# Kernel optimization log

Measured on AMD Instinct MI355X. Metric: run time of the kernel, lower is better.

## Reference

```python
import jax, jax.numpy as jnp
import numpy as np

E_DIM = 64
N_EMBED = 1024
N_TOKENS = 262144


def setup_inputs() -> dict:
    key = jax.random.key(0)
    k1, k2 = jax.random.split(key)
    inp = jax.random.normal(k1, (N_TOKENS, E_DIM), dtype=jnp.float32)
    # codebook init mirrors torch uniform_(-1/n_embed, 1/n_embed)
    embed = jax.random.uniform(k2, (E_DIM, N_EMBED), dtype=jnp.float32,
                               minval=-1.0 / N_EMBED, maxval=1.0 / N_EMBED)
    return {"input": inp, "embed": embed}


def reference(input, embed):
    e_dim, n_embed = embed.shape
    flatten = input.reshape(-1, e_dim)  # [N, e_dim]
    dist = (jnp.sum(flatten * flatten, axis=1, keepdims=True)
            - 2.0 * flatten @ embed
            + jnp.sum(embed * embed, axis=0, keepdims=True))
    embed_idxs = jnp.argmin(dist, axis=1)  # matches (-dist).max(1) indices
    embed_idxs = embed_idxs.reshape(input.shape[:-1])
    quantize = jnp.take(embed.T, embed_idxs, axis=0)  # gather codes -> [..., e_dim]
    # straight-through estimator
    quantize_input_grad = input + jax.lax.stop_gradient(quantize - input)
    return (quantize, input, quantize_input_grad, embed_idxs, embed)
```

## Files before the change

### kernel.cpp

```cpp
#include <hip/hip_runtime.h>
#include <hip/hip_bf16.h>
#include <math.h>

#define E_DIM    64
#define N_EMBED  1024
#define N_TOKENS 262144
#define FQCAP    32768

typedef __attribute__((ext_vector_type(8)))  short bf16x8;
typedef __attribute__((ext_vector_type(16))) float f32x16;


__device__ __forceinline__ short f2bf_bits(float f) {
    __hip_bfloat16 h = __float2bfloat16(f);
    return *reinterpret_cast<short*>(&h);
}
__device__ __forceinline__ float bfbits2f(short s) {
    unsigned int u = ((unsigned int)(unsigned short)s) << 16;
    return __uint_as_float(u);
}

__device__ __forceinline__ float exact_d(const float* __restrict__ xrow,
                                         const float* __restrict__ emb,
                                         const float* __restrict__ csum,
                                         float a, int j) {
#pragma clang fp contract(off)
    float b = 0.f;
#pragma unroll
    for (int k = 0; k < E_DIM; ++k) b = fmaf(xrow[k], emb[k * N_EMBED + j], b);
    return (a - 2.0f * b) + csum[j];
}

__device__ __forceinline__ float a_np_of(const float* x) {
#pragma clang fp contract(off)
    float s[16];
#pragma unroll
    for (int i = 0; i < 16; ++i)
        s[i] = (x[i] * x[i] + x[i + 16] * x[i + 16]) +
               (x[i + 32] * x[i + 32] + x[i + 48] * x[i + 48]);
    float hh[8];
#pragma unroll
    for (int i = 0; i < 8; ++i) hh[i] = s[i] + s[i + 8];
    float uu[4];
#pragma unroll
    for (int i = 0; i < 4; ++i) uu[i] = hh[i] + hh[i + 4];
    return (uu[0] + uu[2]) + (uu[1] + uu[3]);
}

__device__ __forceinline__ bool lexless(float av, int ai, float bv, int bi) {
    return (av < bv) || (av == bv && ai < bi);
}

__global__ __launch_bounds__(256) void vq_prep(const float* __restrict__ emb,
                                               short* __restrict__ eTc,
                                               float* __restrict__ out_e,
                                               float* __restrict__ embT,
                                               float* __restrict__ c_out) {
    const int b = blockIdx.x;
    if (b < 256) {
        const int t = b * 256 + threadIdx.x;
        const int k = t >> 10, n = t & 1023;
        float e = emb[t];
        float m2 = -2.0f * e;
        short hb = f2bf_bits(m2);
        short lb = f2bf_bits(m2 - bfbits2f(hb));
        const int chunk = n >> 7, code = n & 127, slot = k >> 3, jj = k & 7;
        const int base = chunk * 16384 + (slot * 128 + code) * 8 + jj;
        eTc[base]        = hb;
        eTc[base + 8192] = lb;
        out_e[t] = e;
        embT[n * E_DIM + k] = e;
    } else {
#pragma clang fp contract(off)
        const int j = (b - 256) * 256 + threadIdx.x;
        float e = emb[j];
        float s = e * e;
        for (int k = 1; k < E_DIM; ++k) {
            float ek = emb[k * N_EMBED + j];
            float pk = ek * ek;
            s = s + pk;
        }
        c_out[j] = s;
    }
}

__device__ __forceinline__ void tile_epilogue(
    const f32x16& acc, int codebase_global, int h,
    float& v1, float& v2, float& v3, int& i1, int& i2) {
#pragma unroll
    for (int r = 0; r < 16; ++r) {
        const int row = (r & 3) + 8 * (r >> 2) + 4 * h;
        const float d = acc[r];
        const int idx = codebase_global + row;
        if (d < v3) {
            if (d < v1)      { v3 = v2; v2 = v1; i2 = i1; v1 = d; i1 = idx; }
            else if (d < v2) { v3 = v2; v2 = d;  i2 = idx; }
            else             { v3 = d; }
        }
    }
}

__global__ __launch_bounds__(256, 4) void vq_screen_kernel(
    const float* __restrict__ in, const float* __restrict__ emb,
    const float* __restrict__ csum, const short* __restrict__ eTc,
    float* __restrict__ out_idx,
    unsigned int* __restrict__ qcnt, unsigned int* __restrict__ fullQ)
{
    __shared__ uint4 lds_e[2048];

    const int t = threadIdx.x;
    const int wave = t >> 6, l = t & 63, col = l & 31, h = l >> 5;
    const int tok = blockIdx.x * 128 + wave * 32 + col;
    const float* xrow = in + (size_t)tok * E_DIM;

    float xv[4][8];
#pragma unroll
    for (int s = 0; s < 4; ++s) {
        float4 u0 = *reinterpret_cast<const float4*>(xrow + s * 16 + h * 8);
        float4 u1 = *reinterpret_cast<const float4*>(xrow + s * 16 + h * 8 + 4);
        xv[s][0] = u0.x; xv[s][1] = u0.y; xv[s][2] = u0.z; xv[s][3] = u0.w;
        xv[s][4] = u1.x; xv[s][5] = u1.y; xv[s][6] = u1.z; xv[s][7] = u1.w;
    }
    bf16x8 bhi[4], blo[4];
    float sax_h = 0.f;
#pragma unroll
    for (int s = 0; s < 4; ++s) {
#pragma unroll
        for (int j = 0; j < 8; ++j) {
            float x = xv[s][j];
            sax_h += fabsf(x);
            short hb = f2bf_bits(x);
            bhi[s][j] = hb;
            blo[s][j] = f2bf_bits(x - bfbits2f(hb));
        }
    }
    const float sax = sax_h + __shfl_xor(sax_h, 32, 64);

    float a_np;
    {
#pragma clang fp contract(off)
        float sv[8];
#pragma unroll
        for (int j = 0; j < 8; ++j) {
            float p0 = xv[0][j] * xv[0][j];
            float p1 = xv[1][j] * xv[1][j];
            float p2 = xv[2][j] * xv[2][j];
            float p3 = xv[3][j] * xv[3][j];
            sv[j] = (p0 + p1) + (p2 + p3);
        }
        float hh[8];
#pragma unroll
        for (int j = 0; j < 8; ++j) hh[j] = sv[j] + __shfl_xor(sv[j], 32, 64);
        float u0 = hh[0] + hh[4], u1 = hh[1] + hh[5];
        float u2 = hh[2] + hh[6], u3 = hh[3] + hh[7];
        a_np = (u0 + u2) + (u1 + u3);
    }

    float v1 = 3.4e38f, v2 = 3.4e38f, v3 = 3.4e38f;
    int i1 = 0, i2 = 0;

    for (int cc = 0; cc < 8; ++cc) {
        __syncthreads();
        {
            const uint4* gsrc = reinterpret_cast<const uint4*>(eTc) + cc * 2048;
#pragma unroll
            for (int j = 0; j < 8; ++j) lds_e[j * 256 + t] = gsrc[j * 256 + t];
        }
        __syncthreads();

        const int cb = cc << 7;
#pragma unroll
        for (int tp = 0; tp < 2; ++tp) {
            const int c0 = tp * 64 + col;
            const int cbase = cb + tp * 64 + 4 * h;
            const float4 cA0 = *reinterpret_cast<const float4*>(&csum[cbase + 0]);
            const float4 cA1 = *reinterpret_cast<const float4*>(&csum[cbase + 8]);
            const float4 cA2 = *reinterpret_cast<const float4*>(&csum[cbase + 16]);
            const float4 cA3 = *reinterpret_cast<const float4*>(&csum[cbase + 24]);
            const float4 cB0 = *reinterpret_cast<const float4*>(&csum[cbase + 32]);
            const float4 cB1 = *reinterpret_cast<const float4*>(&csum[cbase + 40]);
            const float4 cB2 = *reinterpret_cast<const float4*>(&csum[cbase + 48]);
            const float4 cB3 = *reinterpret_cast<const float4*>(&csum[cbase + 56]);
            f32x16 accA, accB;
            accA[0]=cA0.x;  accA[1]=cA0.y;  accA[2]=cA0.z;  accA[3]=cA0.w;
            accA[4]=cA1.x;  accA[5]=cA1.y;  accA[6]=cA1.z;  accA[7]=cA1.w;
            accA[8]=cA2.x;  accA[9]=cA2.y;  accA[10]=cA2.z; accA[11]=cA2.w;
            accA[12]=cA3.x; accA[13]=cA3.y; accA[14]=cA3.z; accA[15]=cA3.w;
            accB[0]=cB0.x;  accB[1]=cB0.y;  accB[2]=cB0.z;  accB[3]=cB0.w;
            accB[4]=cB1.x;  accB[5]=cB1.y;  accB[6]=cB1.z;  accB[7]=cB1.w;
            accB[8]=cB2.x;  accB[9]=cB2.y;  accB[10]=cB2.z; accB[11]=cB2.w;
            accB[12]=cB3.x; accB[13]=cB3.y; accB[14]=cB3.z; accB[15]=cB3.w;
#pragma unroll
            for (int s = 0; s < 4; ++s) {
                const int slot = 2 * s + h;
                bf16x8 ahA = *reinterpret_cast<const bf16x8*>(&lds_e[slot * 128 + c0]);
                bf16x8 alA = *reinterpret_cast<const bf16x8*>(&lds_e[1024 + slot * 128 + c0]);
                bf16x8 ahB = *reinterpret_cast<const bf16x8*>(&lds_e[slot * 128 + c0 + 32]);
                bf16x8 alB = *reinterpret_cast<const bf16x8*>(&lds_e[1024 + slot * 128 + c0 + 32]);
                accA = __builtin_amdgcn_mfma_f32_32x32x16_bf16(ahA, bhi[s], accA, 0, 0, 0);
                accB = __builtin_amdgcn_mfma_f32_32x32x16_bf16(ahB, bhi[s], accB, 0, 0, 0);
                accA = __builtin_amdgcn_mfma_f32_32x32x16_bf16(ahA, blo[s], accA, 0, 0, 0);
                accB = __builtin_amdgcn_mfma_f32_32x32x16_bf16(ahB, blo[s], accB, 0, 0, 0);
                accA = __builtin_amdgcn_mfma_f32_32x32x16_bf16(alA, bhi[s], accA, 0, 0, 0);
                accB = __builtin_amdgcn_mfma_f32_32x32x16_bf16(alB, bhi[s], accB, 0, 0, 0);
            }
            tile_epilogue(accA, cb + tp * 64,      h, v1, v2, v3, i1, i2);
            tile_epilogue(accB, cb + tp * 64 + 32, h, v1, v2, v3, i1, i2);
        }
    }

    const float w1 = __shfl_xor(v1, 32, 64), w2 = __shfl_xor(v2, 32, 64), w3 = __shfl_xor(v3, 32, 64);
    const int   j1 = __shfl_xor(i1, 32, 64), j2 = __shfl_xor(i2, 32, 64);
    const bool bfirst = lexless(w1, j1, v1, i1);
    const float r1v = bfirst ? w1 : v1;  const int r1i = bfirst ? j1 : i1;
    const float cav = bfirst ? v1 : v2;  const int cai = bfirst ? i1 : i2;
    const float cbv = bfirst ? w2 : w1;  const int cbi = bfirst ? j2 : j1;
    const bool bsec = lexless(cbv, cbi, cav, cai);
    const float r2v = bsec ? cbv : cav;  const int r2i = bsec ? cbi : cai;
    const float r3v = bsec ? fminf(cav, bfirst ? w3 : w2)
                           : fminf(cbv, bfirst ? v2 : v3);

    if (l < 32) {
        const float thr = 8e-5f + 4e-7f * sax;
        const bool sane = (a_np < 150.f) && (sax < 128.f) && (fabsf(r1v) < 0.5f);
        int fin = r1i;
        if (sane && (r2v - r1v > thr)) {
        } else if (sane && (r3v - r1v > thr)) {
            const float d1 = exact_d(xrow, emb, csum, a_np, r1i);
            const float d2 = exact_d(xrow, emb, csum, a_np, r2i);
            if (d2 < d1 || (d2 == d1 && r2i < r1i)) fin = r2i;
        } else {
            const unsigned int qi = atomicAdd(qcnt, 1u);
            if (qi < FQCAP) fullQ[qi] = (unsigned int)tok;
        }
        out_idx[tok] = (float)fin;
    }
}

__global__ __launch_bounds__(256) void vq_full_kernel(
    const float* __restrict__ in, const float* __restrict__ emb,
    const float* __restrict__ csum, const unsigned int* __restrict__ qcnt,
    const unsigned int* __restrict__ fullQ, float* __restrict__ out_idx) {
#pragma clang fp contract(off)
    unsigned int nq = *qcnt;
    if (nq > FQCAP) nq = FQCAP;
    const int l = threadIdx.x & 63;
    for (unsigned int w = blockIdx.x * 4 + (threadIdx.x >> 6); w < nq; w += 1024) {
        const int tok = (int)fullQ[w];
        const float* xrow = in + (size_t)tok * E_DIM;
        float x[E_DIM];
#pragma unroll
        for (int j4 = 0; j4 < 16; ++j4) {
            const float4 u = *reinterpret_cast<const float4*>(xrow + j4 * 4);
            x[j4 * 4 + 0] = u.x; x[j4 * 4 + 1] = u.y;
            x[j4 * 4 + 2] = u.z; x[j4 * 4 + 3] = u.w;
        }
        const float a = a_np_of(x);
        const int c0 = l * 16;
        float b[16];
#pragma unroll
        for (int q = 0; q < 16; ++q) b[q] = 0.f;
        for (int k = 0; k < E_DIM; ++k) {
            const float xk = x[k];
            const float* er = emb + k * N_EMBED + c0;
#pragma unroll
            for (int q = 0; q < 16; ++q) b[q] = fmaf(xk, er[q], b[q]);
        }
        float bd = 3.4e38f; int bi = 1 << 30;
#pragma unroll
        for (int q = 0; q < 16; ++q) {
            const float d = (a - 2.0f * b[q]) + csum[c0 + q];
            if (d < bd) { bd = d; bi = c0 + q; }
        }
        for (int m = 1; m < 64; m <<= 1) {
            const float od = __shfl_xor(bd, m, 64);
            const int oi = __shfl_xor(bi, m, 64);
            if (od < bd || (od == bd && oi < bi)) { bd = od; bi = oi; }
        }
        if (l == 0) out_idx[tok] = (float)bi;
    }
}

__global__ __launch_bounds__(256) void vq_gather_kernel(
    const float* __restrict__ in, const float* __restrict__ embT,
    const float* __restrict__ idxf,
    float* __restrict__ out_q, float* __restrict__ out_in, float* __restrict__ out_g) {
#pragma clang fp contract(off)
    const size_t j = (size_t)blockIdx.x * 256 + threadIdx.x;
    const int m  = (int)(j >> 4);
    const int k0 = ((int)j & 15) * 4;
    const int idx = (int)idxf[m];

    const float4 x = reinterpret_cast<const float4*>(in)[j];
    const float4 q = *reinterpret_cast<const float4*>(&embT[(size_t)idx * E_DIM + k0]);

    float4 g;
    g.x = x.x + (q.x - x.x);
    g.y = x.y + (q.y - x.y);
    g.z = x.z + (q.z - x.z);
    g.w = x.w + (q.w - x.w);

    reinterpret_cast<float4*>(out_q)[j]  = q;
    reinterpret_cast<float4*>(out_in)[j] = x;
    reinterpret_cast<float4*>(out_g)[j]  = g;
}

extern "C" void kernel_launch(void* const* d_in, const int* in_sizes, int n_in,
                              void* d_out, int out_size, void* d_ws, size_t ws_size,
                              hipStream_t stream) {
    const float* in  = (const float*)d_in[0];
    const float* emb = (const float*)d_in[1];

    float* out     = (float*)d_out;
    float* out_q   = out;
    float* out_in  = out + (size_t)N_TOKENS * E_DIM;
    float* out_g   = out + 2ull * N_TOKENS * E_DIM;
    float* out_idx = out + 3ull * N_TOKENS * E_DIM;
    float* out_e   = out_idx + N_TOKENS;

    unsigned char* ws = (unsigned char*)d_ws;
    float*          c_ws  = (float*)(ws);
    short*          eTc   = (short*)(ws + 4096);
    float*          embT  = (float*)(ws + 4096 + 262144);
    unsigned int*   qcnt  = (unsigned int*)(ws + 4096 + 262144 + 262144);
    unsigned int*   fullQ = (unsigned int*)(ws + 4096 + 262144 + 262144 + 256);

    hipMemsetAsync(qcnt, 0, sizeof(unsigned int), stream);

    vq_prep<<<260, 256, 0, stream>>>(emb, eTc, out_e, embT, c_ws);

    vq_screen_kernel<<<N_TOKENS / 128, 256, 0, stream>>>(
        in, emb, c_ws, eTc, out_idx, qcnt, fullQ);

    vq_full_kernel<<<256, 256, 0, stream>>>(in, emb, c_ws, qcnt, fullQ, out_idx);

    const int gather_blocks = (N_TOKENS * E_DIM / 4) / 256;
    vq_gather_kernel<<<gather_blocks, 256, 0, stream>>>(in, embT, out_idx,
                                                        out_q, out_in, out_g);
}
```

Before: 273.7 us.

## Fuse gather/STE output writes into screen kernel and defer pair checks

Removes the separate gather kernel by having the screen kernel write quantize, input copy and straight-through outputs directly from registers using the screened index. Ambiguous two-candidate tokens are now queued to a new pair kernel instead of doing scalar exact checks inline, and the pair and full-rescan kernels overwrite the outputs for tokens they correct. This saves re-reading the input and the index array, at the cost of redundant writes for corrected tokens, an extra launch, and lower occupancy (launch bound 4 to 3).

```diff
diff --git a/kernel.cpp b/kernel.cpp
--- a/kernel.cpp
+++ b/kernel.cpp
@@ -5,6 +5,7 @@
 #define E_DIM    64
 #define N_EMBED  1024
 #define N_TOKENS 262144
+#define PQCAP    32768
 #define FQCAP    32768
 
 typedef __attribute__((ext_vector_type(8)))  short bf16x8;
@@ -18,17 +19,6 @@
 __device__ __forceinline__ float bfbits2f(short s) {
     unsigned int u = ((unsigned int)(unsigned short)s) << 16;
     return __uint_as_float(u);
-}
-
-__device__ __forceinline__ float exact_d(const float* __restrict__ xrow,
-                                         const float* __restrict__ emb,
-                                         const float* __restrict__ csum,
-                                         float a, int j) {
-#pragma clang fp contract(off)
-    float b = 0.f;
-#pragma unroll
-    for (int k = 0; k < E_DIM; ++k) b = fmaf(xrow[k], emb[k * N_EMBED + j], b);
-    return (a - 2.0f * b) + csum[j];
 }
 
 __device__ __forceinline__ float a_np_of(const float* x) {
@@ -100,11 +90,13 @@
     }
 }
 
-__global__ __launch_bounds__(256, 4) void vq_screen_kernel(
-    const float* __restrict__ in, const float* __restrict__ emb,
-    const float* __restrict__ csum, const short* __restrict__ eTc,
-    float* __restrict__ out_idx,
-    unsigned int* __restrict__ qcnt, unsigned int* __restrict__ fullQ)
+__global__ __launch_bounds__(256, 3) void vq_screen_kernel(
+    const float* __restrict__ in, const float* __restrict__ csum,
+    const short* __restrict__ eTc, const float* __restrict__ embT,
+    float* __restrict__ out_idx, float* __restrict__ out_q,
+    float* __restrict__ out_in, float* __restrict__ out_g,
+    unsigned int* __restrict__ qcnt,
+    uint2* __restrict__ pairQ, unsigned int* __restrict__ fullQ)
 {
     __shared__ uint4 lds_e[2048];
 
@@ -220,29 +212,105 @@
     const float r3v = bsec ? fminf(cav, bfirst ? w3 : w2)
                            : fminf(cbv, bfirst ? v2 : v3);
 
+    const float thr = 8e-5f + 4e-7f * sax;
+    const bool sane = (a_np < 150.f) && (sax < 128.f) && (fabsf(r1v) < 0.5f);
+    const int fin = r1i;
+
     if (l < 32) {
-        const float thr = 8e-5f + 4e-7f * sax;
-        const bool sane = (a_np < 150.f) && (sax < 128.f) && (fabsf(r1v) < 0.5f);
-        int fin = r1i;
         if (sane && (r2v - r1v > thr)) {
         } else if (sane && (r3v - r1v > thr)) {
-            const float d1 = exact_d(xrow, emb, csum, a_np, r1i);
-            const float d2 = exact_d(xrow, emb, csum, a_np, r2i);
-            if (d2 < d1 || (d2 == d1 && r2i < r1i)) fin = r2i;
+            const unsigned int qi = atomicAdd(&qcnt[0], 1u);
+            if (qi < PQCAP)
+                pairQ[qi] = make_uint2((unsigned int)tok,
+                                       (unsigned int)r1i | ((unsigned int)r2i << 16));
         } else {
-            const unsigned int qi = atomicAdd(qcnt, 1u);
+            const unsigned int qi = atomicAdd(&qcnt[1], 1u);
             if (qi < FQCAP) fullQ[qi] = (unsigned int)tok;
         }
         out_idx[tok] = (float)fin;
+    }
+
+    {
+        const float* qrow = embT + (size_t)fin * E_DIM;
+        const size_t obase = (size_t)tok * E_DIM;
+#pragma unroll
+        for (int s = 0; s < 4; ++s) {
+            const int k0 = s * 16 + h * 8;
+            const float4 q0 = *reinterpret_cast<const float4*>(qrow + k0);
+            const float4 q1 = *reinterpret_cast<const float4*>(qrow + k0 + 4);
+            const float4 x0 = make_float4(xv[s][0], xv[s][1], xv[s][2], xv[s][3]);
+            const float4 x1 = make_float4(xv[s][4], xv[s][5], xv[s][6], xv[s][7]);
+            float4 g0, g1;
+            g0.x = x0.x + (q0.x - x0.x); g0.y = x0.y + (q0.y - x0.y);
+            g0.z = x0.z + (q0.z - x0.z); g0.w = x0.w + (q0.w - x0.w);
+            g1.x = x1.x + (q1.x - x1.x); g1.y = x1.y + (q1.y - x1.y);
+            g1.z = x1.z + (q1.z - x1.z); g1.w = x1.w + (q1.w - x1.w);
+            *reinterpret_cast<float4*>(out_q  + obase + k0)     = q0;
+            *reinterpret_cast<float4*>(out_q  + obase + k0 + 4) = q1;
+            *reinterpret_cast<float4*>(out_in + obase + k0)     = x0;
+            *reinterpret_cast<float4*>(out_in + obase + k0 + 4) = x1;
+            *reinterpret_cast<float4*>(out_g  + obase + k0)     = g0;
+            *reinterpret_cast<float4*>(out_g  + obase + k0 + 4) = g1;
+        }
+    }
+}
+
+__global__ __launch_bounds__(256) void vq_pair_kernel(
+    const float* __restrict__ in, const float* __restrict__ emb,
+    const float* __restrict__ embT, const float* __restrict__ csum,
+    const unsigned int* __restrict__ qcnt, const uint2* __restrict__ pairQ,
+    float* __restrict__ out_idx, float* __restrict__ out_q,
+    float* __restrict__ out_g) {
+#pragma clang fp contract(off)
+    unsigned int nq = qcnt[0];
+    if (nq > PQCAP) nq = PQCAP;
+    const unsigned int i = blockIdx.x * 256 + threadIdx.x;
+    if (i >= nq) return;
+    const uint2 e = pairQ[i];
+    const int tok = (int)e.x;
+    const int c1 = (int)(e.y & 0xFFFFu), c2 = (int)(e.y >> 16);
+    const float* xrow = in + (size_t)tok * E_DIM;
+    float x[E_DIM];
+#pragma unroll
+    for (int j4 = 0; j4 < 16; ++j4) {
+        const float4 u = *reinterpret_cast<const float4*>(xrow + j4 * 4);
+        x[j4 * 4 + 0] = u.x; x[j4 * 4 + 1] = u.y;
+        x[j4 * 4 + 2] = u.z; x[j4 * 4 + 3] = u.w;
+    }
+    const float a = a_np_of(x);
+    float b1 = 0.f, b2 = 0.f;
+#pragma unroll
+    for (int k = 0; k < E_DIM; ++k) {
+        b1 = fmaf(x[k], emb[k * N_EMBED + c1], b1);
+        b2 = fmaf(x[k], emb[k * N_EMBED + c2], b2);
+    }
+    const float d1 = (a - 2.0f * b1) + csum[c1];
+    const float d2 = (a - 2.0f * b2) + csum[c2];
+    const int fin = (d2 < d1 || (d2 == d1 && c2 < c1)) ? c2 : c1;
+    out_idx[tok] = (float)fin;
+    const float* qrow = embT + (size_t)fin * E_DIM;
+    const size_t obase = (size_t)tok * E_DIM;
+#pragma unroll
+    for (int j4 = 0; j4 < 16; ++j4) {
+        const float4 q = *reinterpret_cast<const float4*>(qrow + j4 * 4);
+        float4 g;
+        g.x = x[j4 * 4 + 0] + (q.x - x[j4 * 4 + 0]);
+        g.y = x[j4 * 4 + 1] + (q.y - x[j4 * 4 + 1]);
+        g.z = x[j4 * 4 + 2] + (q.z - x[j4 * 4 + 2]);
+        g.w = x[j4 * 4 + 3] + (q.w - x[j4 * 4 + 3]);
+        *reinterpret_cast<float4*>(out_q + obase + j4 * 4) = q;
+        *reinterpret_cast<float4*>(out_g + obase + j4 * 4) = g;
     }
 }
 
 __global__ __launch_bounds__(256) void vq_full_kernel(
     const float* __restrict__ in, const float* __restrict__ emb,
-    const float* __restrict__ csum, const unsigned int* __restrict__ qcnt,
-    const unsigned int* __restrict__ fullQ, float* __restrict__ out_idx) {
-#pragma clang fp contract(off)
-    unsigned int nq = *qcnt;
+    const float* __restrict__ embT, const float* __restrict__ csum,
+    const unsigned int* __restrict__ qcnt, const unsigned int* __restrict__ fullQ,
+    float* __restrict__ out_idx, float* __restrict__ out_q,
+    float* __restrict__ out_g) {
+#pragma clang fp contract(off)
+    unsigned int nq = qcnt[1];
     if (nq > FQCAP) nq = FQCAP;
     const int l = threadIdx.x & 63;
     for (unsigned int w = blockIdx.x * 4 + (threadIdx.x >> 6); w < nq; w += 1024) {
@@ -278,31 +346,18 @@
             if (od < bd || (od == bd && oi < bi)) { bd = od; bi = oi; }
         }
         if (l == 0) out_idx[tok] = (float)bi;
-    }
-}
-
-__global__ __launch_bounds__(256) void vq_gather_kernel(
-    const float* __restrict__ in, const float* __restrict__ embT,
-    const float* __restrict__ idxf,
-    float* __restrict__ out_q, float* __restrict__ out_in, float* __restrict__ out_g) {
-#pragma clang fp contract(off)
-    const size_t j = (size_t)blockIdx.x * 256 + threadIdx.x;
-    const int m  = (int)(j >> 4);
-    const int k0 = ((int)j & 15) * 4;
-    const int idx = (int)idxf[m];
-
-    const float4 x = reinterpret_cast<const float4*>(in)[j];
-    const float4 q = *reinterpret_cast<const float4*>(&embT[(size_t)idx * E_DIM + k0]);
-
-    float4 g;
-    g.x = x.x + (q.x - x.x);
-    g.y = x.y + (q.y - x.y);
-    g.z = x.z + (q.z - x.z);
-    g.w = x.w + (q.w - x.w);
-
-    reinterpret_cast<float4*>(out_q)[j]  = q;
-    reinterpret_cast<float4*>(out_in)[j] = x;
-    reinterpret_cast<float4*>(out_g)[j]  = g;
+        if (l < 16) {
+            const float4 qv = *reinterpret_cast<const float4*>(embT + (size_t)bi * E_DIM + l * 4);
+            const float4 xq = *reinterpret_cast<const float4*>(xrow + l * 4);
+            float4 g;
+            g.x = xq.x + (qv.x - xq.x);
+            g.y = xq.y + (qv.y - xq.y);
+            g.z = xq.z + (qv.z - xq.z);
+            g.w = xq.w + (qv.w - xq.w);
+            *reinterpret_cast<float4*>(out_q + (size_t)tok * E_DIM + l * 4) = qv;
+            *reinterpret_cast<float4*>(out_g + (size_t)tok * E_DIM + l * 4) = g;
+        }
+    }
 }
 
 extern "C" void kernel_launch(void* const* d_in, const int* in_sizes, int n_in,
@@ -323,18 +378,20 @@
     short*          eTc   = (short*)(ws + 4096);
     float*          embT  = (float*)(ws + 4096 + 262144);
     unsigned int*   qcnt  = (unsigned int*)(ws + 4096 + 262144 + 262144);
-    unsigned int*   fullQ = (unsigned int*)(ws + 4096 + 262144 + 262144 + 256);
-
-    hipMemsetAsync(qcnt, 0, sizeof(unsigned int), stream);
+    uint2*          pairQ = (uint2*)(ws + 4096 + 262144 + 262144 + 256);
+    unsigned int*   fullQ = (unsigned int*)(ws + 4096 + 262144 + 262144 + 256
+                                            + (size_t)PQCAP * 8);
+
+    hipMemsetAsync(qcnt, 0, 2 * sizeof(unsigned int), stream);
 
     vq_prep<<<260, 256, 0, stream>>>(emb, eTc, out_e, embT, c_ws);
 
     vq_screen_kernel<<<N_TOKENS / 128, 256, 0, stream>>>(
-        in, emb, c_ws, eTc, out_idx, qcnt, fullQ);
-
-    vq_full_kernel<<<256, 256, 0, stream>>>(in, emb, c_ws, qcnt, fullQ, out_idx);
-
-    const int gather_blocks = (N_TOKENS * E_DIM / 4) / 256;
-    vq_gather_kernel<<<gather_blocks, 256, 0, stream>>>(in, embT, out_idx,
-                                                        out_q, out_in, out_g);
-}
+        in, c_ws, eTc, embT, out_idx, out_q, out_in, out_g, qcnt, pairQ, fullQ);
+
+    vq_pair_kernel<<<PQCAP / 256, 256, 0, stream>>>(
+        in, emb, embT, c_ws, qcnt, pairQ, out_idx, out_q, out_g);
+
+    vq_full_kernel<<<256, 256, 0, stream>>>(
+        in, emb, embT, c_ws, qcnt, fullQ, out_idx, out_q, out_g);
+}
```

Result: slower. 306.6 us (+12.0%).

## Fuse gather and straight-through outputs into screen and fallback kernels

Applied to the files above, without the earlier changes.

Removes the separate gather kernel and writes the input copy, quantized codes and straight-through gradient directly from the screening kernel using the x values already held in registers. The fallback full-search kernel then overwrites the quantized and gradient rows for the tokens it re-resolves. This avoids re-reading the input and the index array and saves a kernel launch. In exchange the screen kernel gains register pressure and stores, and queued tokens are written twice, with ordering between the two kernels relied on for correctness.

```diff
diff --git a/kernel.cpp b/kernel.cpp
--- a/kernel.cpp
+++ b/kernel.cpp
@@ -103,7 +103,9 @@
 __global__ __launch_bounds__(256, 4) void vq_screen_kernel(
     const float* __restrict__ in, const float* __restrict__ emb,
     const float* __restrict__ csum, const short* __restrict__ eTc,
-    float* __restrict__ out_idx,
+    const float* __restrict__ embT,
+    float* __restrict__ out_idx, float* __restrict__ out_q,
+    float* __restrict__ out_in, float* __restrict__ out_g,
     unsigned int* __restrict__ qcnt, unsigned int* __restrict__ fullQ)
 {
     __shared__ uint4 lds_e[2048];
@@ -112,6 +114,7 @@
     const int wave = t >> 6, l = t & 63, col = l & 31, h = l >> 5;
     const int tok = blockIdx.x * 128 + wave * 32 + col;
     const float* xrow = in + (size_t)tok * E_DIM;
+    const size_t obase = (size_t)tok * E_DIM;
 
     float xv[4][8];
 #pragma unroll
@@ -121,6 +124,16 @@
         xv[s][0] = u0.x; xv[s][1] = u0.y; xv[s][2] = u0.z; xv[s][3] = u0.w;
         xv[s][4] = u1.x; xv[s][5] = u1.y; xv[s][6] = u1.z; xv[s][7] = u1.w;
     }
+
+#pragma unroll
+    for (int s = 0; s < 4; ++s) {
+        const int k0 = s * 16 + h * 8;
+        *reinterpret_cast<float4*>(out_in + obase + k0) =
+            make_float4(xv[s][0], xv[s][1], xv[s][2], xv[s][3]);
+        *reinterpret_cast<float4*>(out_in + obase + k0 + 4) =
+            make_float4(xv[s][4], xv[s][5], xv[s][6], xv[s][7]);
+    }
+
     bf16x8 bhi[4], blo[4];
     float sax_h = 0.f;
 #pragma unroll
@@ -220,27 +233,48 @@
     const float r3v = bsec ? fminf(cav, bfirst ? w3 : w2)
                            : fminf(cbv, bfirst ? v2 : v3);
 
-    if (l < 32) {
-        const float thr = 8e-5f + 4e-7f * sax;
-        const bool sane = (a_np < 150.f) && (sax < 128.f) && (fabsf(r1v) < 0.5f);
-        int fin = r1i;
-        if (sane && (r2v - r1v > thr)) {
-        } else if (sane && (r3v - r1v > thr)) {
-            const float d1 = exact_d(xrow, emb, csum, a_np, r1i);
-            const float d2 = exact_d(xrow, emb, csum, a_np, r2i);
-            if (d2 < d1 || (d2 == d1 && r2i < r1i)) fin = r2i;
-        } else {
+    const float thr = 8e-5f + 4e-7f * sax;
+    const bool sane = (a_np < 150.f) && (sax < 128.f) && (fabsf(r1v) < 0.5f);
+    int fin = r1i;
+    if (sane && (r2v - r1v > thr)) {
+    } else if (sane && (r3v - r1v > thr)) {
+        const float d1 = exact_d(xrow, emb, csum, a_np, r1i);
+        const float d2 = exact_d(xrow, emb, csum, a_np, r2i);
+        if (d2 < d1 || (d2 == d1 && r2i < r1i)) fin = r2i;
+    } else {
+        if (l < 32) {
             const unsigned int qi = atomicAdd(qcnt, 1u);
             if (qi < FQCAP) fullQ[qi] = (unsigned int)tok;
         }
-        out_idx[tok] = (float)fin;
+    }
+    if (l < 32) out_idx[tok] = (float)fin;
+
+    {
+        const float* qrow = embT + (size_t)fin * E_DIM;
+#pragma unroll
+        for (int s = 0; s < 4; ++s) {
+            const int k0 = s * 16 + h * 8;
+            const float4 q0 = *reinterpret_cast<const float4*>(qrow + k0);
+            const float4 q1 = *reinterpret_cast<const float4*>(qrow + k0 + 4);
+            float4 g0, g1;
+            g0.x = xv[s][0] + (q0.x - xv[s][0]); g0.y = xv[s][1] + (q0.y - xv[s][1]);
+            g0.z = xv[s][2] + (q0.z - xv[s][2]); g0.w = xv[s][3] + (q0.w - xv[s][3]);
+            g1.x = xv[s][4] + (q1.x - xv[s][4]); g1.y = xv[s][5] + (q1.y - xv[s][5]);
+            g1.z = xv[s][6] + (q1.z - xv[s][6]); g1.w = xv[s][7] + (q1.w - xv[s][7]);
+            *reinterpret_cast<float4*>(out_q + obase + k0)     = q0;
+            *reinterpret_cast<float4*>(out_q + obase + k0 + 4) = q1;
+            *reinterpret_cast<float4*>(out_g + obase + k0)     = g0;
+            *reinterpret_cast<float4*>(out_g + obase + k0 + 4) = g1;
+        }
     }
 }
 
 __global__ __launch_bounds__(256) void vq_full_kernel(
     const float* __restrict__ in, const float* __restrict__ emb,
-    const float* __restrict__ csum, const unsigned int* __restrict__ qcnt,
-    const unsigned int* __restrict__ fullQ, float* __restrict__ out_idx) {
+    const float* __restrict__ embT, const float* __restrict__ csum,
+    const unsigned int* __restrict__ qcnt, const unsigned int* __restrict__ fullQ,
+    float* __restrict__ out_idx, float* __restrict__ out_q,
+    float* __restrict__ out_g) {
 #pragma clang fp contract(off)
     unsigned int nq = *qcnt;
     if (nq > FQCAP) nq = FQCAP;
@@ -278,31 +312,18 @@
             if (od < bd || (od == bd && oi < bi)) { bd = od; bi = oi; }
         }
         if (l == 0) out_idx[tok] = (float)bi;
-    }
-}
-
-__global__ __launch_bounds__(256) void vq_gather_kernel(
-    const float* __restrict__ in, const float* __restrict__ embT,
-    const float* __restrict__ idxf,
-    float* __restrict__ out_q, float* __restrict__ out_in, float* __restrict__ out_g) {
-#pragma clang fp contract(off)
-    const size_t j = (size_t)blockIdx.x * 256 + threadIdx.x;
-    const int m  = (int)(j >> 4);
-    const int k0 = ((int)j & 15) * 4;
-    const int idx = (int)idxf[m];
-
-    const float4 x = reinterpret_cast<const float4*>(in)[j];
-    const float4 q = *reinterpret_cast<const float4*>(&embT[(size_t)idx * E_DIM + k0]);
-
-    float4 g;
-    g.x = x.x + (q.x - x.x);
-    g.y = x.y + (q.y - x.y);
-    g.z = x.z + (q.z - x.z);
-    g.w = x.w + (q.w - x.w);
-
-    reinterpret_cast<float4*>(out_q)[j]  = q;
-    reinterpret_cast<float4*>(out_in)[j] = x;
-    reinterpret_cast<float4*>(out_g)[j]  = g;
+        if (l < 16) {
+            const float4 qv = *reinterpret_cast<const float4*>(embT + (size_t)bi * E_DIM + l * 4);
+            const float4 xq = *reinterpret_cast<const float4*>(xrow + l * 4);
+            float4 g;
+            g.x = xq.x + (qv.x - xq.x);
+            g.y = xq.y + (qv.y - xq.y);
+            g.z = xq.z + (qv.z - xq.z);
+            g.w = xq.w + (qv.w - xq.w);
+            *reinterpret_cast<float4*>(out_q + (size_t)tok * E_DIM + l * 4) = qv;
+            *reinterpret_cast<float4*>(out_g + (size_t)tok * E_DIM + l * 4) = g;
+        }
+    }
 }
 
 extern "C" void kernel_launch(void* const* d_in, const int* in_sizes, int n_in,
@@ -330,11 +351,8 @@
     vq_prep<<<260, 256, 0, stream>>>(emb, eTc, out_e, embT, c_ws);
 
     vq_screen_kernel<<<N_TOKENS / 128, 256, 0, stream>>>(
-        in, emb, c_ws, eTc, out_idx, qcnt, fullQ);
-
-    vq_full_kernel<<<256, 256, 0, stream>>>(in, emb, c_ws, qcnt, fullQ, out_idx);
-
-    const int gather_blocks = (N_TOKENS * E_DIM / 4) / 256;
-    vq_gather_kernel<<<gather_blocks, 256, 0, stream>>>(in, embT, out_idx,
-                                                        out_q, out_in, out_g);
-}
+        in, emb, c_ws, eTc, embT, out_idx, out_q, out_in, out_g, qcnt, fullQ);
+
+    vq_full_kernel<<<256, 256, 0, stream>>>(
+        in, emb, embT, c_ws, qcnt, fullQ, out_idx, out_q, out_g);
+}
```

Result: slower. 320.6 us (+17.1%).
